# Performance work log

Hardware: AMD Instinct MI355X
Metric: run time of the kernel (lower is better)

Reference implementation:

```python
import jax, jax.numpy as jnp
import numpy as np

NUM_BLOCKS = 4      # config.num_target_blocks
SCALE_MIN = 0.15    # config.target_scale_min
SCALE_MAX = 0.2     # config.target_scale_max
ASPECT = 1.0        # config.target_aspect_ratio


def setup_inputs() -> dict:
    key = jax.random.key(0)
    k1, k2, k3 = jax.random.split(key, 3)
    batch_size, height, width = 8192, 64, 64
    seq_len = height * width
    tb = batch_size * NUM_BLOCKS
    return {
        "scales": jax.random.uniform(k1, (tb,), jnp.float32),
        "rand_tops": jax.random.uniform(k2, (tb,), jnp.float32),
        "rand_lefts": jax.random.uniform(k3, (tb,), jnp.float32),
        "batch_size": batch_size,
        "seq_len": seq_len,
        "height": height,
        "width": width,
    }


def _target_mask(scales, rand_tops, rand_lefts, batch_size, seq_len, height, width):
    # scale in [SCALE_MIN, SCALE_MAX) -> integer block area (torch .int() truncates)
    s = SCALE_MIN + scales * (SCALE_MAX - SCALE_MIN)
    area = (s * height * width).astype(jnp.int32)  # [TB]
    # block_h = clamp(int(sqrt(area / aspect)), 1, H)
    bh = jnp.clip(jnp.sqrt(area.astype(jnp.float32) / ASPECT).astype(jnp.int32), 1, height)
    # block_w = clamp(int(area / block_h), 1, W)  (torch int/int is true-div then trunc)
    bw = jnp.clip((area.astype(jnp.float32) / bh.astype(jnp.float32)).astype(jnp.int32), 1, width)
    max_tops = jnp.maximum(height - bh + 1, 1)
    max_lefts = jnp.maximum(width - bw + 1, 1)
    tops = (rand_tops * max_tops.astype(jnp.float32)).astype(jnp.int32)
    lefts = (rand_lefts * max_lefts.astype(jnp.float32)).astype(jnp.int32)
    # vectorized rectangle membership, replaces the per-block python loop
    r = jnp.arange(height, dtype=jnp.int32)[None, :]   # [1,H]
    c = jnp.arange(width, dtype=jnp.int32)[None, :]    # [1,W]
    in_row = (r >= tops[:, None]) & (r < (tops + bh)[:, None])     # [TB,H]
    in_col = (c >= lefts[:, None]) & (c < (lefts + bw)[:, None])   # [TB,W]
    block = in_row[:, :, None] & in_col[:, None, :]                # [TB,H,W]
    # row-major flatten == positions rows*width+cols; keep positions < seq_len
    block = block.reshape(block.shape[0], height * width)[:, :seq_len]
    # OR together the NUM_BLOCKS rectangles per batch element
    target = jnp.any(block.reshape(batch_size, NUM_BLOCKS, seq_len), axis=1)
    return target  # [B, seq_len] bool


def reference(scales, rand_tops, rand_lefts, batch_size, seq_len, height, width):
    target_mask = _target_mask(scales, rand_tops, rand_lefts,
                               batch_size, seq_len, height, width)
    context_mask = ~target_mask
    # ragged target_positions list -> jit-friendly padded form:
    # stable argsort puts True positions (in ascending index order) first;
    # counts[b] gives how many leading entries are valid.
    positions = jnp.argsort(~target_mask, axis=1, stable=True)
    counts = target_mask.sum(axis=1, dtype=jnp.int32)
    return context_mask, target_mask, positions, counts
```

## Files before the change

### kernel.cpp

```cpp
#include <hip/hip_runtime.h>


#define NBLK 4
#define HGT 64
#define WID 64
#define SEQ 4096

__global__ __launch_bounds__(256) void blockmask_kernel(
    const float* __restrict__ scales,
    const float* __restrict__ rand_tops,
    const float* __restrict__ rand_lefts,
    int* __restrict__ out,
    int B)
{
    __shared__ int pos_s[SEQ];
    __shared__ int wsum[4];

    const int b   = blockIdx.x;
    const int tid = threadIdx.x;

    int top[NBLK], bot[NBLK], lft[NBLK], rgt[NBLK];
#pragma unroll
    for (int j = 0; j < NBLK; ++j) {
        int t = b * NBLK + j;
        float sc = scales[t];
        float s = __fadd_rn(0.15f, __fmul_rn(sc, 0.05f));
        int area = (int)__fmul_rn(__fmul_rn(s, 64.0f), 64.0f);
        int bh = (int)__fsqrt_rn((float)area);
        bh = min(max(bh, 1), HGT);
        int bw = (int)__fdiv_rn((float)area, (float)bh);
        bw = min(max(bw, 1), WID);
        int maxt = max(HGT - bh + 1, 1);
        int maxl = max(WID - bw + 1, 1);
        int tp = (int)__fmul_rn(rand_tops[t],  (float)maxt);
        int lf = (int)__fmul_rn(rand_lefts[t], (float)maxl);
        top[j] = tp; bot[j] = tp + bh;
        lft[j] = lf; rgt[j] = lf + bw;
    }

    const int p0 = tid * 16;
    const int r  = p0 >> 6;
    const int c0 = p0 & 63;

    unsigned mask16 = 0;
#pragma unroll
    for (int j = 0; j < NBLK; ++j) {
        if (r >= top[j] && r < bot[j]) {
            int lo = max(lft[j] - c0, 0);
            int hi = min(rgt[j] - c0, 16);
            if (hi > lo) mask16 |= ((1u << (hi - lo)) - 1u) << lo;
        }
    }
    const int cnt = __popc(mask16);

    const int lane = tid & 63;
    const int wv   = tid >> 6;
    int v = cnt;
#pragma unroll
    for (int d = 1; d < 64; d <<= 1) {
        int t = __shfl_up(v, d, 64);
        if (lane >= d) v += t;
    }
    if (lane == 63) wsum[wv] = v;
    __syncthreads();
    int waveOff = 0, total = 0;
#pragma unroll
    for (int w = 0; w < 4; ++w) {
        int ws = wsum[w];
        if (w < wv) waveOff += ws;
        total += ws;
    }
    const int base_t = waveOff + (v - cnt);

    int bt = base_t;
    int bn = total + (p0 - base_t);
#pragma unroll
    for (int k = 0; k < 16; ++k) {
        int p = p0 + k;
        if ((mask16 >> k) & 1u) pos_s[bt++] = p;
        else                    pos_s[bn++] = p;
    }

    const size_t BS = (size_t)B * SEQ;
    int4* ctx4 = (int4*)out        + (size_t)b * (SEQ / 4);
    int4* tgt4 = (int4*)(out + BS) + (size_t)b * (SEQ / 4);
#pragma unroll
    for (int g = 0; g < 4; ++g) {
        int vidx = g * 256 + tid;
        int p  = vidx * 4;
        int rr = p >> 6;
        int cc = p & 63;
        int m = 0;
#pragma unroll
        for (int j = 0; j < NBLK; ++j) {
            if (rr >= top[j] && rr < bot[j]) {
                int lo = max(lft[j] - cc, 0);
                int hi = min(rgt[j] - cc, 4);
                if (hi > lo) m |= ((1 << (hi - lo)) - 1) << lo;
            }
        }
        int4 tv, cv;
        tv.x =  m       & 1; tv.y = (m >> 1) & 1; tv.z = (m >> 2) & 1; tv.w = (m >> 3) & 1;
        cv.x = tv.x ^ 1;     cv.y = tv.y ^ 1;     cv.z = tv.z ^ 1;     cv.w = tv.w ^ 1;
        tgt4[vidx] = tv;
        ctx4[vidx] = cv;
    }

    __syncthreads();
    const int4* ps4 = (const int4*)pos_s;
    int4* pout4 = (int4*)(out + 2 * BS) + (size_t)b * (SEQ / 4);
#pragma unroll
    for (int g = 0; g < 4; ++g) {
        int vidx = g * 256 + tid;
        pout4[vidx] = ps4[vidx];
    }

    if (tid == 0) out[3 * BS + (size_t)b] = total;
}

extern "C" void kernel_launch(void* const* d_in, const int* in_sizes, int n_in,
                              void* d_out, int out_size, void* d_ws, size_t ws_size,
                              hipStream_t stream) {
    const float* scales     = (const float*)d_in[0];
    const float* rand_tops  = (const float*)d_in[1];
    const float* rand_lefts = (const float*)d_in[2];
    int* out = (int*)d_out;
    int B = in_sizes[0] / NBLK;
    blockmask_kernel<<<B, 256, 0, stream>>>(scales, rand_tops, rand_lefts, out, B);
}
```

Measured before the change: 402.5 us.

## Precompute packed rectangles in a prepass and use 64-bit column masks

Splits the per-rectangle parameter computation into a separate small kernel that packs top/bottom/left/right into one 32-bit word in workspace, so each block loads a single uint4 instead of recomputing sqrt/div per thread. Row membership now ORs precomputed 64-bit column masks instead of per-rectangle range arithmetic. The scatter into shared memory uses popcount-derived addresses instead of sequential counters. This adds an extra kernel launch and a workspace round trip, and the main kernel stays bound by its output writes.

```diff
diff --git a/kernel.cpp b/kernel.cpp
--- a/kernel.cpp
+++ b/kernel.cpp
@@ -6,12 +6,38 @@
 #define WID 64
 #define SEQ 4096
 
-__global__ __launch_bounds__(256) void blockmask_kernel(
+__device__ __forceinline__ unsigned pack_rect(float sc, float rt, float rl) {
+    float s = __fadd_rn(0.15f, __fmul_rn(sc, 0.05f));
+    int area = (int)__fmul_rn(__fmul_rn(s, 64.0f), 64.0f);
+    int bh = (int)__fsqrt_rn((float)area);
+    bh = min(max(bh, 1), HGT);
+    int bw = (int)__fdiv_rn((float)area, (float)bh);
+    bw = min(max(bw, 1), WID);
+    int maxt = max(HGT - bh + 1, 1);
+    int maxl = max(WID - bw + 1, 1);
+    int tp = (int)__fmul_rn(rt, (float)maxt);
+    int lf = (int)__fmul_rn(rl, (float)maxl);
+    return (unsigned)tp | ((unsigned)(tp + bh) << 8)
+         | ((unsigned)lf << 16) | ((unsigned)(lf + bw) << 24);
+}
+
+__global__ __launch_bounds__(256) void bm_params(
     const float* __restrict__ scales,
     const float* __restrict__ rand_tops,
     const float* __restrict__ rand_lefts,
-    int* __restrict__ out,
-    int B)
+    unsigned int* __restrict__ rects, int TB)
+{
+    int t = blockIdx.x * 256 + threadIdx.x;
+    if (t < TB) rects[t] = pack_rect(scales[t], rand_tops[t], rand_lefts[t]);
+}
+
+template <bool USE_WS>
+__global__ __launch_bounds__(256) void bm_main(
+    const float* __restrict__ scales,
+    const float* __restrict__ rand_tops,
+    const float* __restrict__ rand_lefts,
+    const uint4* __restrict__ rects4,
+    int* __restrict__ out, int B)
 {
     __shared__ int pos_s[SEQ];
     __shared__ int wsum[4];
@@ -19,38 +45,39 @@
     const int b   = blockIdx.x;
     const int tid = threadIdx.x;
 
-    int top[NBLK], bot[NBLK], lft[NBLK], rgt[NBLK];
+    unsigned rv[NBLK];
+    if (USE_WS) {
+        uint4 rp = rects4[b];
+        rv[0] = rp.x; rv[1] = rp.y; rv[2] = rp.z; rv[3] = rp.w;
+    } else {
+#pragma unroll
+        for (int j = 0; j < NBLK; ++j) {
+            int t = b * NBLK + j;
+            rv[j] = pack_rect(scales[t], rand_tops[t], rand_lefts[t]);
+        }
+    }
+
+    int top[NBLK], bot[NBLK];
+    unsigned long long cmask[NBLK];
 #pragma unroll
     for (int j = 0; j < NBLK; ++j) {
-        int t = b * NBLK + j;
-        float sc = scales[t];
-        float s = __fadd_rn(0.15f, __fmul_rn(sc, 0.05f));
-        int area = (int)__fmul_rn(__fmul_rn(s, 64.0f), 64.0f);
-        int bh = (int)__fsqrt_rn((float)area);
-        bh = min(max(bh, 1), HGT);
-        int bw = (int)__fdiv_rn((float)area, (float)bh);
-        bw = min(max(bw, 1), WID);
-        int maxt = max(HGT - bh + 1, 1);
-        int maxl = max(WID - bw + 1, 1);
-        int tp = (int)__fmul_rn(rand_tops[t],  (float)maxt);
-        int lf = (int)__fmul_rn(rand_lefts[t], (float)maxl);
-        top[j] = tp; bot[j] = tp + bh;
-        lft[j] = lf; rgt[j] = lf + bw;
+        unsigned v = rv[j];
+        top[j] = (int)(v & 0xffu);
+        bot[j] = (int)((v >> 8) & 0xffu);
+        int lf = (int)((v >> 16) & 0xffu);
+        int bw = (int)((v >> 24) & 0xffu) - lf;
+        unsigned long long m = (bw >= 64) ? ~0ull : ((1ull << bw) - 1ull);
+        cmask[j] = m << lf;
     }
 
     const int p0 = tid * 16;
     const int r  = p0 >> 6;
     const int c0 = p0 & 63;
-
-    unsigned mask16 = 0;
+    unsigned long long rm = 0ull;
 #pragma unroll
-    for (int j = 0; j < NBLK; ++j) {
-        if (r >= top[j] && r < bot[j]) {
-            int lo = max(lft[j] - c0, 0);
-            int hi = min(rgt[j] - c0, 16);
-            if (hi > lo) mask16 |= ((1u << (hi - lo)) - 1u) << lo;
-        }
-    }
+    for (int j = 0; j < NBLK; ++j)
+        if (r >= top[j] && r < bot[j]) rm |= cmask[j];
+    const unsigned mask16 = (unsigned)(rm >> c0) & 0xffffu;
     const int cnt = __popc(mask16);
 
     const int lane = tid & 63;
@@ -72,13 +99,13 @@
     }
     const int base_t = waveOff + (v - cnt);
 
-    int bt = base_t;
-    int bn = total + (p0 - base_t);
 #pragma unroll
     for (int k = 0; k < 16; ++k) {
-        int p = p0 + k;
-        if ((mask16 >> k) & 1u) pos_s[bt++] = p;
-        else                    pos_s[bn++] = p;
+        int tpre = __popc(mask16 & ((1u << k) - 1u));
+        int a_t  = base_t + tpre;
+        int a_n  = total + (p0 - base_t) + (k - tpre);
+        int addr = ((mask16 >> k) & 1u) ? a_t : a_n;
+        pos_s[addr] = p0 + k;
     }
 
     const size_t BS = (size_t)B * SEQ;
@@ -90,18 +117,15 @@
         int p  = vidx * 4;
         int rr = p >> 6;
         int cc = p & 63;
-        int m = 0;
+        unsigned long long rmg = 0ull;
 #pragma unroll
-        for (int j = 0; j < NBLK; ++j) {
-            if (rr >= top[j] && rr < bot[j]) {
-                int lo = max(lft[j] - cc, 0);
-                int hi = min(rgt[j] - cc, 4);
-                if (hi > lo) m |= ((1 << (hi - lo)) - 1) << lo;
-            }
-        }
+        for (int j = 0; j < NBLK; ++j)
+            if (rr >= top[j] && rr < bot[j]) rmg |= cmask[j];
+        int m4 = (int)((rmg >> cc) & 0xfull);
         int4 tv, cv;
-        tv.x =  m       & 1; tv.y = (m >> 1) & 1; tv.z = (m >> 2) & 1; tv.w = (m >> 3) & 1;
-        cv.x = tv.x ^ 1;     cv.y = tv.y ^ 1;     cv.z = tv.z ^ 1;     cv.w = tv.w ^ 1;
+        tv.x =  m4       & 1; tv.y = (m4 >> 1) & 1;
+        tv.z = (m4 >> 2) & 1; tv.w = (m4 >> 3) & 1;
+        cv.x = tv.x ^ 1; cv.y = tv.y ^ 1; cv.z = tv.z ^ 1; cv.w = tv.w ^ 1;
         tgt4[vidx] = tv;
         ctx4[vidx] = cv;
     }
@@ -125,6 +149,16 @@
     const float* rand_tops  = (const float*)d_in[1];
     const float* rand_lefts = (const float*)d_in[2];
     int* out = (int*)d_out;
-    int B = in_sizes[0] / NBLK;
-    blockmask_kernel<<<B, 256, 0, stream>>>(scales, rand_tops, rand_lefts, out, B);
+    const int TB = in_sizes[0];
+    const int B  = TB / NBLK;
+
+    if (ws_size >= (size_t)TB * sizeof(unsigned int)) {
+        unsigned int* rects = (unsigned int*)d_ws;
+        bm_params<<<(TB + 255) / 256, 256, 0, stream>>>(scales, rand_tops, rand_lefts, rects, TB);
+        bm_main<true><<<B, 256, 0, stream>>>(scales, rand_tops, rand_lefts,
+                                             (const uint4*)rects, out, B);
+    } else {
+        bm_main<false><<<B, 256, 0, stream>>>(scales, rand_tops, rand_lefts,
+                                              nullptr, out, B);
+    }
 }
```

After: 405.7 us. Within noise of the previous version (+0.8%).
